# Optimization experiments

Hardware: AMD Instinct MI355X
Metric: run time of the kernel (lower is better)

## Reference

```python
import jax, jax.numpy as jnp
import numpy as np

HEADS = 16


def setup_inputs() -> dict:
    key = jax.random.key(0)
    k1, k2, k3, k4 = jax.random.split(key, 4)
    C, T, E = 8, 4096, 1024
    D = E // HEADS
    x = jax.random.normal(k1, (C, T, E), dtype=jnp.float32)
    # nn.Linear(per_dim, per_dim, bias=False) weights, stored [out, in] as in torch
    Wq = jax.random.normal(k2, (D, D), dtype=jnp.float32) * (1.0 / np.sqrt(D))
    Wk = jax.random.normal(k3, (D, D), dtype=jnp.float32) * (1.0 / np.sqrt(D))
    Wv = jax.random.normal(k4, (D, D), dtype=jnp.float32) * (1.0 / np.sqrt(D))
    return {"x": x, "Wq": Wq, "Wk": Wk, "Wv": Wv}


def reference(x, Wq, Wk, Wv):
    # Faithful to the torch module, including its quirks:
    #  - softmax over dim=0 (the C axis), NOT over keys
    #  - einsum 'ctth,ckhd->cthd' takes the t==q DIAGONAL of the score tensor
    #    and sums values over all positions k.
    # Since softmax over C is pointwise in (t, q, h), softmax(scores)[c,t,t,h]
    # == softmax(diag_scores)[c,t,h], so we never materialize the T x T tensor.
    C, T, E = x.shape
    H = HEADS
    D = E // H
    xr = x.reshape(C, T, H, D)
    q = jnp.einsum('cthd,ed->cthe', xr, Wq)  # Linear: x @ W.T
    k = jnp.einsum('cthd,ed->cthe', xr, Wk)
    v = jnp.einsum('cthd,ed->cthe', xr, Wv)
    diag_scores = jnp.einsum('cthd,cthd->cth', q, k) / jnp.sqrt(jnp.asarray(E, x.dtype))
    probs = jax.nn.softmax(diag_scores, axis=0)  # softmax over C, as in torch dim=0
    vsum = v.sum(axis=1)  # [C, H, D], sum over key positions k
    attn = probs[..., None] * vsum[:, None, :, :]  # [C, T, H, D]
    return attn.reshape(C, T, E)
```

## Files before the change

kernel.cpp:

```cpp
#include <hip/hip_runtime.h>
#include <hip/hip_bf16.h>

#define CC 8
#define TT 4096
#define EE 1024
#define HH 16
#define DD 64
#define TOKB 32
#define TBLK (TT / TOKB)
#define OT 8

typedef __attribute__((ext_vector_type(8))) short short8;
typedef __attribute__((ext_vector_type(4))) float f32x4;

static __device__ __forceinline__ short f2bf(float f) {
    unsigned u = __builtin_bit_cast(unsigned, f);
    u += 0x7fff + ((u >> 16) & 1);
    return (short)(u >> 16);
}

static __device__ __forceinline__ f32x4 mfma16(short8 a, short8 b, f32x4 c) {
    return __builtin_amdgcn_mfma_f32_16x16x32_bf16(a, b, c, 0, 0, 0);
}

__global__ __launch_bounds__(256, 2)
void k1_scores(const float* __restrict__ x, const float* __restrict__ Wq,
               const float* __restrict__ Wk, float* __restrict__ s_out,
               float* __restrict__ part_out) {
    const int bid = blockIdx.x;
    const int c = bid >> 7, tb = bid & (TBLK - 1);
    const int tid = threadIdx.x;
    const int w = tid >> 6;
    const int lane = tid & 63;
    const int lg = lane >> 4;
    const int lr = lane & 15;

    __shared__ short fragW[16][512];
    __shared__ float red[4][1024];

    for (int rep = 0; rep < 4; ++rep) {
        int slot = rep * 256 + tid;
        int f = slot >> 6, ln = slot & 63;
        int which = f >> 3, et = (f >> 1) & 3, kc = f & 1;
        const float* Wp = which ? Wk : Wq;
        const float* src = Wp + (et * 16 + (ln & 15)) * 64 + kc * 32 + (ln >> 4) * 8;
        short8 v;
        #pragma unroll
        for (int j = 0; j < 8; ++j) v[j] = f2bf(src[j]);
        *reinterpret_cast<short8*>(&fragW[f][ln * 8]) = v;
    }
    __syncthreads();

    const float* xbase = x + (size_t)(c * TT + tb * TOKB) * EE;
    f32x4 xa0 = {0,0,0,0}, xa1 = {0,0,0,0}, xa2 = {0,0,0,0}, xa3 = {0,0,0,0};

    for (int it = 0; it < TOKB / 4; ++it) {
        const int tloc = it * 4 + w;
        const float* tp = xbase + (size_t)tloc * EE + lr * 64 + lg * 8;
        f32x4 f0 = *(const f32x4*)(tp);
        f32x4 f1 = *(const f32x4*)(tp + 4);
        f32x4 f2 = *(const f32x4*)(tp + 32);
        f32x4 f3 = *(const f32x4*)(tp + 36);
        xa0 += f0; xa1 += f1; xa2 += f2; xa3 += f3;

        short8 a0, a1;
        #pragma unroll
        for (int j = 0; j < 4; ++j) { a0[j] = f2bf(f0[j]); a0[j+4] = f2bf(f1[j]); }
        #pragma unroll
        for (int j = 0; j < 4; ++j) { a1[j] = f2bf(f2[j]); a1[j+4] = f2bf(f3[j]); }

        float p0 = 0.f, p1 = 0.f, p2 = 0.f, p3 = 0.f;
        #pragma unroll
        for (int et = 0; et < 4; ++et) {
            short8 bq0 = *(const short8*)&fragW[et * 2 + 0][lane * 8];
            short8 bq1 = *(const short8*)&fragW[et * 2 + 1][lane * 8];
            f32x4 qa = {0,0,0,0};
            qa = mfma16(a0, bq0, qa);
            qa = mfma16(a1, bq1, qa);
            short8 bk0 = *(const short8*)&fragW[8 + et * 2 + 0][lane * 8];
            short8 bk1 = *(const short8*)&fragW[8 + et * 2 + 1][lane * 8];
            f32x4 ka = {0,0,0,0};
            ka = mfma16(a0, bk0, ka);
            ka = mfma16(a1, bk1, ka);
            p0 += qa[0] * ka[0]; p1 += qa[1] * ka[1];
            p2 += qa[2] * ka[2]; p3 += qa[3] * ka[3];
        }
        #pragma unroll
        for (int m = 1; m < 16; m <<= 1) {
            p0 += __shfl_xor(p0, m);
            p1 += __shfl_xor(p1, m);
            p2 += __shfl_xor(p2, m);
            p3 += __shfl_xor(p3, m);
        }
        if (lr == 0) {
            const float inv = 1.0f / 32.0f;
            int t = tb * TOKB + tloc;
            f32x4 sv = { p0 * inv, p1 * inv, p2 * inv, p3 * inv };
            *(f32x4*)&s_out[((size_t)c * TT + t) * HH + lg * 4] = sv;
        }
    }

    {
        int base = lr * 64 + lg * 8;
        *(f32x4*)&red[w][base + 0]  = xa0;
        *(f32x4*)&red[w][base + 4]  = xa1;
        *(f32x4*)&red[w][base + 32] = xa2;
        *(f32x4*)&red[w][base + 36] = xa3;
    }
    __syncthreads();
    float* pb = part_out + (size_t)bid * 1024;
    #pragma unroll
    for (int k = 0; k < 4; ++k) {
        int slot = k * 256 + tid;
        pb[slot] = red[0][slot] + red[1][slot] + red[2][slot] + red[3][slot];
    }
}

__global__ __launch_bounds__(256)
void k2_vsum(const float* __restrict__ part, const float* __restrict__ Wv,
             float* __restrict__ vsum) {
    const int b = blockIdx.x;
    const int c = b >> 4, h = b & 15;
    const int tid = threadIdx.x;
    __shared__ float xs[4][64];
    __shared__ float xsum[64];

    const int d = tid & 63, g = tid >> 6;
    float a = 0.f;
    for (int tb = g * 32; tb < g * 32 + 32; ++tb)
        a += part[(size_t)(c * TBLK + tb) * 1024 + h * 64 + d];
    xs[g][d] = a;
    __syncthreads();
    if (tid < 64) xsum[tid] = xs[0][tid] + xs[1][tid] + xs[2][tid] + xs[3][tid];
    __syncthreads();
    if (tid < 64) {
        const float* wr = Wv + tid * 64;
        float acc = 0.f;
        #pragma unroll 16
        for (int dd = 0; dd < 64; ++dd) acc += wr[dd] * xsum[dd];
        vsum[(size_t)c * 1024 + h * 64 + tid] = acc;
    }
}

__global__ __launch_bounds__(256)
void k3_out(const float* __restrict__ s_in, const float* __restrict__ vsum,
            float* __restrict__ out) {
    const int b = blockIdx.x;
    const int tid = threadIdx.x;
    __shared__ float lv[CC * 1024];
    __shared__ float ls[CC][OT * HH];

    #pragma unroll
    for (int r = 0; r < 8; ++r) {
        int idx = r * 1024 + tid * 4;
        *(f32x4*)&lv[idx] = *(const f32x4*)&vsum[idx];
    }
    const int t0 = b * OT;
    if (tid < OT * HH) {
        #pragma unroll
        for (int c = 0; c < CC; ++c)
            ls[c][tid] = s_in[((size_t)c * TT + t0) * HH + tid];
    }
    __syncthreads();
    if (tid < OT * HH) {
        float v[CC], m = -1e30f;
        #pragma unroll
        for (int c = 0; c < CC; ++c) { v[c] = ls[c][tid]; m = fmaxf(m, v[c]); }
        float sum = 0.f;
        #pragma unroll
        for (int c = 0; c < CC; ++c) { v[c] = expf(v[c] - m); sum += v[c]; }
        float r = 1.0f / sum;
        #pragma unroll
        for (int c = 0; c < CC; ++c) ls[c][tid] = v[c] * r;
    }
    __syncthreads();
    const int h = tid >> 4;
    #pragma unroll
    for (int c = 0; c < CC; ++c) {
        f32x4 vv = *(f32x4*)&lv[c * 1024 + tid * 4];
        #pragma unroll
        for (int t = 0; t < OT; ++t) {
            float p = ls[c][t * HH + h];
            f32x4 o = { vv[0] * p, vv[1] * p, vv[2] * p, vv[3] * p };
            *(f32x4*)&out[((size_t)c * TT + t0 + t) * EE + tid * 4] = o;
        }
    }
}

extern "C" void kernel_launch(void* const* d_in, const int* in_sizes, int n_in,
                              void* d_out, int out_size, void* d_ws, size_t ws_size,
                              hipStream_t stream) {
    const float* x  = (const float*)d_in[0];
    const float* Wq = (const float*)d_in[1];
    const float* Wk = (const float*)d_in[2];
    const float* Wv = (const float*)d_in[3];
    float* out = (float*)d_out;
    float* ws  = (float*)d_ws;

    float* s    = ws;
    float* part = ws + 524288;
    float* vsum = ws + 524288 + 1024 * 1024;

    k1_scores<<<CC * TBLK, 256, 0, stream>>>(x, Wq, Wk, s, part);
    k2_vsum  <<<CC * HH,   256, 0, stream>>>(part, Wv, vsum);
    k3_out   <<<TT / OT,   256, 0, stream>>>(s, vsum, out);
}
```

Measured before the change: 261.3 us.

## Prefetch x with nontemporal loads, drop LDS staging in output kernel

k1 now software-prefetches the next token's x slice with nontemporal loads while computing the current one, and its occupancy hint goes from 2 to 3 blocks. k3 keeps vsum in registers instead of staging 32KB in LDS, reads scores directly from global, uses fast __expf, and writes output with nontemporal stores. k2's partial-sum loop is unrolled and the bf16 conversion uses the library intrinsic. These target memory latency and cache pollution in what is a bandwidth-bound pipeline, at the cost of more registers and slightly lower-precision exp.

```diff
diff --git a/kernel.cpp b/kernel.cpp
--- a/kernel.cpp
+++ b/kernel.cpp
@@ -5,7 +5,6 @@
 #define TT 4096
 #define EE 1024
 #define HH 16
-#define DD 64
 #define TOKB 32
 #define TBLK (TT / TOKB)
 #define OT 8
@@ -14,16 +13,19 @@
 typedef __attribute__((ext_vector_type(4))) float f32x4;
 
 static __device__ __forceinline__ short f2bf(float f) {
-    unsigned u = __builtin_bit_cast(unsigned, f);
-    u += 0x7fff + ((u >> 16) & 1);
-    return (short)(u >> 16);
+    __hip_bfloat16 h = __float2bfloat16(f);
+    return __builtin_bit_cast(short, h);
+}
+
+static __device__ __forceinline__ f32x4 ldnt(const float* p) {
+    return __builtin_nontemporal_load((const f32x4*)p);
 }
 
 static __device__ __forceinline__ f32x4 mfma16(short8 a, short8 b, f32x4 c) {
     return __builtin_amdgcn_mfma_f32_16x16x32_bf16(a, b, c, 0, 0, 0);
 }
 
-__global__ __launch_bounds__(256, 2)
+__global__ __launch_bounds__(256, 3)
 void k1_scores(const float* __restrict__ x, const float* __restrict__ Wq,
                const float* __restrict__ Wk, float* __restrict__ s_out,
                float* __restrict__ part_out) {
@@ -51,16 +53,25 @@
     }
     __syncthreads();
 
-    const float* xbase = x + (size_t)(c * TT + tb * TOKB) * EE;
+    const float* tp = x + (size_t)(c * TT + tb * TOKB + w) * EE + lr * 64 + lg * 8;
     f32x4 xa0 = {0,0,0,0}, xa1 = {0,0,0,0}, xa2 = {0,0,0,0}, xa3 = {0,0,0,0};
 
+    f32x4 f0 = ldnt(tp);
+    f32x4 f1 = ldnt(tp + 4);
+    f32x4 f2 = ldnt(tp + 32);
+    f32x4 f3 = ldnt(tp + 36);
+
+    #pragma unroll
     for (int it = 0; it < TOKB / 4; ++it) {
-        const int tloc = it * 4 + w;
-        const float* tp = xbase + (size_t)tloc * EE + lr * 64 + lg * 8;
-        f32x4 f0 = *(const f32x4*)(tp);
-        f32x4 f1 = *(const f32x4*)(tp + 4);
-        f32x4 f2 = *(const f32x4*)(tp + 32);
-        f32x4 f3 = *(const f32x4*)(tp + 36);
+        f32x4 g0, g1, g2, g3;
+        if (it + 1 < TOKB / 4) {
+            const float* np = tp + (size_t)(it + 1) * 4 * EE;
+            g0 = ldnt(np);
+            g1 = ldnt(np + 4);
+            g2 = ldnt(np + 32);
+            g3 = ldnt(np + 36);
+        }
+
         xa0 += f0; xa1 += f1; xa2 += f2; xa3 += f3;
 
         short8 a0, a1;
@@ -94,10 +105,11 @@
         }
         if (lr == 0) {
             const float inv = 1.0f / 32.0f;
-            int t = tb * TOKB + tloc;
+            int t = tb * TOKB + it * 4 + w;
             f32x4 sv = { p0 * inv, p1 * inv, p2 * inv, p3 * inv };
             *(f32x4*)&s_out[((size_t)c * TT + t) * HH + lg * 4] = sv;
         }
+        f0 = g0; f1 = g1; f2 = g2; f3 = g3;
     }
 
     {
@@ -127,6 +139,7 @@
 
     const int d = tid & 63, g = tid >> 6;
     float a = 0.f;
+    #pragma unroll 8
     for (int tb = g * 32; tb < g * 32 + 32; ++tb)
         a += part[(size_t)(c * TBLK + tb) * 1024 + h * 64 + d];
     xs[g][d] = a;
@@ -142,47 +155,44 @@
     }
 }
 
-__global__ __launch_bounds__(256)
+__global__ __launch_bounds__(256, 4)
 void k3_out(const float* __restrict__ s_in, const float* __restrict__ vsum,
             float* __restrict__ out) {
     const int b = blockIdx.x;
     const int tid = threadIdx.x;
-    __shared__ float lv[CC * 1024];
+    const int t0 = b * OT;
     __shared__ float ls[CC][OT * HH];
 
-    #pragma unroll
-    for (int r = 0; r < 8; ++r) {
-        int idx = r * 1024 + tid * 4;
-        *(f32x4*)&lv[idx] = *(const f32x4*)&vsum[idx];
-    }
-    const int t0 = b * OT;
-    if (tid < OT * HH) {
-        #pragma unroll
-        for (int c = 0; c < CC; ++c)
-            ls[c][tid] = s_in[((size_t)c * TT + t0) * HH + tid];
-    }
-    __syncthreads();
+    f32x4 vv[CC];
+    #pragma unroll
+    for (int c = 0; c < CC; ++c)
+        vv[c] = *(const f32x4*)&vsum[c * 1024 + tid * 4];
+
     if (tid < OT * HH) {
         float v[CC], m = -1e30f;
         #pragma unroll
-        for (int c = 0; c < CC; ++c) { v[c] = ls[c][tid]; m = fmaxf(m, v[c]); }
+        for (int c = 0; c < CC; ++c) {
+            v[c] = s_in[((size_t)c * TT + t0) * HH + tid];
+            m = fmaxf(m, v[c]);
+        }
         float sum = 0.f;
         #pragma unroll
-        for (int c = 0; c < CC; ++c) { v[c] = expf(v[c] - m); sum += v[c]; }
+        for (int c = 0; c < CC; ++c) { v[c] = __expf(v[c] - m); sum += v[c]; }
         float r = 1.0f / sum;
         #pragma unroll
         for (int c = 0; c < CC; ++c) ls[c][tid] = v[c] * r;
     }
     __syncthreads();
+
     const int h = tid >> 4;
     #pragma unroll
     for (int c = 0; c < CC; ++c) {
-        f32x4 vv = *(f32x4*)&lv[c * 1024 + tid * 4];
+        f32x4 vvc = vv[c];
         #pragma unroll
         for (int t = 0; t < OT; ++t) {
             float p = ls[c][t * HH + h];
-            f32x4 o = { vv[0] * p, vv[1] * p, vv[2] * p, vv[3] * p };
-            *(f32x4*)&out[((size_t)c * TT + t0 + t) * EE + tid * 4] = o;
+            f32x4 o = { vvc[0] * p, vvc[1] * p, vvc[2] * p, vvc[3] * p };
+            __builtin_nontemporal_store(o, (f32x4*)&out[((size_t)c * TT + t0 + t) * EE + tid * 4]);
         }
     }
 }
```

Result: no change. 264.7 us (+1.3%).
